# Kernel optimization log

Measured on AMD Instinct MI355X. Metric: run time of the kernel, lower is better.

## Reference

```python
import jax, jax.numpy as jnp
import numpy as np

NUM_HEADS = 16
HEAD_DIM = 64


def setup_inputs() -> dict:
    key = jax.random.key(0)
    ks = jax.random.split(key, 6)
    B, S, E = 4, 1024, 1024
    return {
        "x": jax.random.normal(ks[0], (B, S, E), dtype=jnp.float32),
        "W_qkv": jax.random.normal(ks[1], (E, 3 * E), dtype=jnp.float32) * 0.02,
        "b_qkv": jax.random.normal(ks[2], (3 * E,), dtype=jnp.float32) * 0.02,
        "pe": jax.random.normal(ks[3], (S, S, HEAD_DIM), dtype=jnp.float32) * 0.02,
        "W_out": jax.random.normal(ks[4], (E, E), dtype=jnp.float32) * 0.02,
        "b_out": jax.random.normal(ks[5], (E,), dtype=jnp.float32) * 0.02,
    }


def reference(x, W_qkv, b_qkv, pe, W_out, b_out):
    B, S, E = x.shape
    H, D = NUM_HEADS, HEAD_DIM
    scale = D ** -0.5
    # qkv projection: (B,S,3E) -> (3,B,H,S,D)
    qkv = (x @ W_qkv + b_qkv).reshape(B, S, 3, H, D).transpose(2, 0, 3, 1, 4)
    q, k, v = qkv[0], qkv[1], qkv[2]
    # raw scaled scores (NO softmax in original module)
    scores = jnp.einsum('bhxd,bhyd->bhxy', q, k) * scale
    # relative position bias: pe is (S,S,D) == (x,y,c); original permutes to (c,x,y)
    # then einsum('cxy,bnxc->bnxy', pe, q) -> equivalent to 'xyc,bhxc->bhxy'
    pe_q = jnp.einsum('xyc,bhxc->bhxy', pe, q) * scale
    attn = (scores + pe_q) @ v                      # (B,H,S,D)
    out = attn.transpose(0, 2, 1, 3).reshape(B, S, E)
    return out @ W_out + b_out
```

## Files before the change

### kernel.cpp

```cpp
#include <hip/hip_runtime.h>
#include <cstdint>
#include <cstddef>


typedef unsigned short u16;
typedef unsigned char  u8;
typedef __bf16 bf16x8 __attribute__((ext_vector_type(8)));
typedef float  f32x4  __attribute__((ext_vector_type(4)));
typedef unsigned short u16x8 __attribute__((ext_vector_type(8)));

#define MFMA16(a, b, c) __builtin_amdgcn_mfma_f32_16x16x32_bf16((a), (b), (c), 0, 0, 0)

#define GLOAD16(g, l)                                                        \
    __builtin_amdgcn_global_load_lds(                                        \
        (const __attribute__((address_space(1))) unsigned int*)(g),          \
        (__attribute__((address_space(3))) unsigned int*)(l), 16, 0, 0)

__device__ __forceinline__ u16 f2bf(float f) {
    __bf16 h = (__bf16)f;
    return __builtin_bit_cast(u16, h);
}
__device__ __forceinline__ u16x8 pack8(float4 a, float4 b) {
    u16x8 v;
    v[0] = f2bf(a.x); v[1] = f2bf(a.y); v[2] = f2bf(a.z); v[3] = f2bf(a.w);
    v[4] = f2bf(b.x); v[5] = f2bf(b.y); v[6] = f2bf(b.z); v[7] = f2bf(b.w);
    return v;
}

__device__ __forceinline__ void convT_tile(const float* __restrict__ in,
                                           u16* __restrict__ out, int R, int C,
                                           int bx, int by, float (*tile)[68]) {
    const int t  = threadIdx.x;
    const int r0 = by * 64, c0 = bx * 64;
    const int rr = t >> 4, c4 = t & 15;
    for (int p = 0; p < 4; ++p) {
        int r = rr + p * 16;
        float4 v = *(const float4*)&in[(size_t)(r0 + r) * C + c0 + c4 * 4];
        *(float4*)&tile[r][c4 * 4] = v;
    }
    __syncthreads();
    for (int p = 0; p < 4; ++p) {
        int n = rr + p * 16;
        ushort4 o;
        o.x = f2bf(tile[c4 * 4 + 0][n]);
        o.y = f2bf(tile[c4 * 4 + 1][n]);
        o.z = f2bf(tile[c4 * 4 + 2][n]);
        o.w = f2bf(tile[c4 * 4 + 3][n]);
        *(ushort4*)&out[(size_t)(c0 + n) * R + r0 + c4 * 4] = o;
    }
}

__global__ __launch_bounds__(256) void kprep(const float* __restrict__ x,
                                             u16* __restrict__ xb,
                                             const float* __restrict__ Wqkv,
                                             u16* __restrict__ wqkvT,
                                             const float* __restrict__ Wout,
                                             u16* __restrict__ woutT) {
    __shared__ float tile[64][68];
    const int bid = blockIdx.x;
    if (bid < 2048) {
        int i = (bid * 256 + threadIdx.x) * 8;
        float4 f0 = *(const float4*)&x[i];
        float4 f1 = *(const float4*)&x[i + 4];
        *(u16x8*)&xb[i] = pack8(f0, f1);
    } else if (bid < 2816) {
        int r = bid - 2048;
        convT_tile(Wqkv, wqkvT, 1024, 3072, r % 48, r / 48, tile);
    } else {
        int r = bid - 2816;
        convT_tile(Wout, woutT, 1024, 1024, r % 16, r / 16, tile);
    }
}

__global__ __launch_bounds__(256, 2) void kgemm_qkv(const u16* __restrict__ A,
                                                    const u16* __restrict__ WT,
                                                    const float* __restrict__ bias,
                                                    u16* __restrict__ qb,
                                                    u16* __restrict__ kb,
                                                    u16* __restrict__ vtb) {
    __shared__ u16 a_s[128 * 64];
    __shared__ u16 b_s[128 * 64];
    const int t = threadIdx.x;
    const int m0 = blockIdx.y * 128, n0 = blockIdx.x * 128;
    const int lane = t & 63, w = t >> 6, lm = lane & 15, lq = lane >> 4;
    const int mb = (w >> 1) * 64, nb = (w & 1) * 64;
    const int sr = t >> 3, sc = (t & 7) * 8;

    f32x4 acc[4][4] = {};
    for (int k0 = 0; k0 < 1024; k0 += 64) {
        __syncthreads();
#pragma unroll
        for (int p = 0; p < 4; ++p) {
            GLOAD16(&A [(size_t)(m0 + p * 32 + sr) * 1024 + k0 + sc], &a_s[p * 2048 + t * 8]);
            GLOAD16(&WT[(size_t)(n0 + p * 32 + sr) * 1024 + k0 + sc], &b_s[p * 2048 + t * 8]);
        }
        __syncthreads();
#pragma unroll
        for (int ks = 0; ks < 2; ++ks) {
            bf16x8 af[4], bfr[4];
#pragma unroll
            for (int mt = 0; mt < 4; ++mt)
                af[mt] = *(const bf16x8*)&a_s[(mb + mt * 16 + lm) * 64 + ks * 32 + lq * 8];
#pragma unroll
            for (int nt = 0; nt < 4; ++nt)
                bfr[nt] = *(const bf16x8*)&b_s[(nb + nt * 16 + lm) * 64 + ks * 32 + lq * 8];
#pragma unroll
            for (int mt = 0; mt < 4; ++mt)
#pragma unroll
                for (int nt = 0; nt < 4; ++nt)
                    acc[mt][nt] = MFMA16(af[mt], bfr[nt], acc[mt][nt]);
        }
    }
    for (int nt = 0; nt < 4; ++nt) {
        int col = n0 + nb + nt * 16 + lm;
        float bv = bias[col];
        int which = col >> 10;
        int h = (col >> 6) & 15, d = col & 63;
        for (int mt = 0; mt < 4; ++mt) {
            int row0 = m0 + mb + mt * 16 + lq * 4;
            int b = row0 >> 10, s = row0 & 1023;
            if (which == 2) {
                ushort4 o;
                o.x = f2bf(acc[mt][nt][0] + bv);
                o.y = f2bf(acc[mt][nt][1] + bv);
                o.z = f2bf(acc[mt][nt][2] + bv);
                o.w = f2bf(acc[mt][nt][3] + bv);
                *(ushort4*)&vtb[((size_t)(b * 16 + h) * 64 + d) * 1024 + s] = o;
            } else {
                u16* dst = (which == 0) ? qb : kb;
                for (int i = 0; i < 4; ++i)
                    dst[((size_t)((b * 16 + h) * 1024 + s + i)) * 64 + d] =
                        f2bf(acc[mt][nt][i] + bv);
            }
        }
    }
}

__global__ __launch_bounds__(256, 4) void kpq(const u16* __restrict__ qb,
                                              const float* __restrict__ pe,
                                              u8* __restrict__ Pq) {
    __shared__ u16 q_s[64 * 64];
    __shared__ u16 pe_s[64 * 80];
    __shared__ unsigned int o_s[64 * 17];
    const int x = blockIdx.x;
    const int t = threadIdx.x;
    const int lane = t & 63, w = t >> 6, lm = lane & 15, lq = lane >> 4;
#pragma unroll
    for (int p = 0; p < 2; ++p)
        GLOAD16(&qb[(size_t)((p * 32 + (t >> 3)) * 1024 + x) * 64 + (t & 7) * 8],
                &q_s[p * 2048 + t * 8]);
    const int yl = t >> 2, cq = (t & 3) * 16;
    const float* pex = pe + (size_t)x * 65536;
    float4 r0, r1, r2, r3;
    {
        const float* src = &pex[(size_t)yl * 64 + cq];
        r0 = *(const float4*)&src[0];  r1 = *(const float4*)&src[4];
        r2 = *(const float4*)&src[8];  r3 = *(const float4*)&src[12];
    }
    const int obh = t >> 2, oyc = t & 3;
    for (int it = 0; it < 16; ++it) {
        *(u16x8*)&pe_s[yl * 80 + cq]     = pack8(r0, r1);
        *(u16x8*)&pe_s[yl * 80 + cq + 8] = pack8(r2, r3);
        __syncthreads();
        if (it < 15) {
            const float* src = &pex[(size_t)((it + 1) * 64 + yl) * 64 + cq];
            r0 = *(const float4*)&src[0];  r1 = *(const float4*)&src[4];
            r2 = *(const float4*)&src[8];  r3 = *(const float4*)&src[12];
        }
        f32x4 acc[4] = {};
#pragma unroll
        for (int ks = 0; ks < 2; ++ks) {
            bf16x8 a = *(const bf16x8*)&pe_s[(16 * w + lm) * 80 + ks * 32 + lq * 8];
#pragma unroll
            for (int nt = 0; nt < 4; ++nt) {
                bf16x8 b = *(const bf16x8*)&q_s[(nt * 16 + lm) * 64 + ks * 32 + lq * 8];
                acc[nt] = MFMA16(a, b, acc[nt]);
            }
        }
#pragma unroll
        for (int nt = 0; nt < 4; ++nt) {
            unsigned int pw;
            pw = __builtin_amdgcn_cvt_pk_fp8_f32(acc[nt][0], acc[nt][1], 0u, false);
            pw = __builtin_amdgcn_cvt_pk_fp8_f32(acc[nt][2], acc[nt][3], pw, true);
            o_s[(nt * 16 + lm) * 17 + 4 * w + lq] = pw;
        }
        __syncthreads();
        uint4 dv;
        dv.x = o_s[obh * 17 + oyc * 4 + 0];
        dv.y = o_s[obh * 17 + oyc * 4 + 1];
        dv.z = o_s[obh * 17 + oyc * 4 + 2];
        dv.w = o_s[obh * 17 + oyc * 4 + 3];
        *(uint4*)&Pq[((size_t)obh * 1024 + x) * 1024 + it * 64 + oyc * 16] = dv;
    }
}

__global__ __launch_bounds__(256, 2) void kattn(const u16* __restrict__ qb,
                                                const u16* __restrict__ kb,
                                                const u16* __restrict__ vt,
                                                const u8* __restrict__ Pq,
                                                u16* __restrict__ attnb) {
    __shared__ u16 q_s[128 * 64];
    __shared__ u16 k_s[64 * 64];
    __shared__ u16 v_s[64 * 64];
    __shared__ u16 s_s[128 * 80];
    const int bid = blockIdx.x;
    const int bh = bid & 63, x0 = (bid >> 6) * 128;
    const int t = threadIdx.x;
    const int lane = t & 63, w = t >> 6, lm = lane & 15, lq = lane >> 4;
    const int sr = t >> 3, sc = (t & 7) * 8;

#pragma unroll
    for (int p = 0; p < 4; ++p)
        GLOAD16(&qb[(size_t)(bh * 1024 + x0 + p * 32 + sr) * 64 + sc],
                &q_s[p * 2048 + t * 8]);

    const u8* PqRow = Pq + ((size_t)(bh * 1024) + x0 + 32 * w + lm) * 1024 + lq * 4;
    f32x4 oacc[2][4] = {};
    for (int y0 = 0; y0 < 1024; y0 += 64) {
        unsigned int pqr[4][2];
#pragma unroll
        for (int nt = 0; nt < 2; ++nt)
#pragma unroll
            for (int mt = 0; mt < 4; ++mt)
                pqr[mt][nt] = *(const unsigned int*)&PqRow[(size_t)(nt * 16) * 1024 + y0 + mt * 16];
        __syncthreads();
#pragma unroll
        for (int p = 0; p < 2; ++p) {
            GLOAD16(&kb[(size_t)(bh * 1024 + y0 + p * 32 + sr) * 64 + sc],
                    &k_s[p * 2048 + t * 8]);
            GLOAD16(&vt[(size_t)(bh * 64 + p * 32 + sr) * 1024 + y0 + sc],
                    &v_s[p * 2048 + t * 8]);
        }
        __syncthreads();
        f32x4 sacc[4][2] = {};
#pragma unroll
        for (int ks = 0; ks < 2; ++ks) {
            bf16x8 bq[2];
#pragma unroll
            for (int nt = 0; nt < 2; ++nt)
                bq[nt] = *(const bf16x8*)&q_s[(32 * w + nt * 16 + lm) * 64 + ks * 32 + lq * 8];
#pragma unroll
            for (int mt = 0; mt < 4; ++mt) {
                bf16x8 ak = *(const bf16x8*)&k_s[(mt * 16 + lm) * 64 + ks * 32 + lq * 8];
#pragma unroll
                for (int nt = 0; nt < 2; ++nt)
                    sacc[mt][nt] = MFMA16(ak, bq[nt], sacc[mt][nt]);
            }
        }
#pragma unroll
        for (int nt = 0; nt < 2; ++nt) {
            int xl = 32 * w + nt * 16 + lm;
#pragma unroll
            for (int mt = 0; mt < 4; ++mt) {
                unsigned int pw = pqr[mt][nt];
                ushort4 o;
                o.x = f2bf((sacc[mt][nt][0] + __builtin_amdgcn_cvt_f32_fp8(pw, 0)) * 0.125f);
                o.y = f2bf((sacc[mt][nt][1] + __builtin_amdgcn_cvt_f32_fp8(pw, 1)) * 0.125f);
                o.z = f2bf((sacc[mt][nt][2] + __builtin_amdgcn_cvt_f32_fp8(pw, 2)) * 0.125f);
                o.w = f2bf((sacc[mt][nt][3] + __builtin_amdgcn_cvt_f32_fp8(pw, 3)) * 0.125f);
                *(ushort4*)&s_s[xl * 80 + mt * 16 + lq * 4] = o;
            }
        }
#pragma unroll
        for (int ks = 0; ks < 2; ++ks) {
            bf16x8 as[2];
#pragma unroll
            for (int mt = 0; mt < 2; ++mt)
                as[mt] = *(const bf16x8*)&s_s[(32 * w + mt * 16 + lm) * 80 + ks * 32 + lq * 8];
#pragma unroll
            for (int nt = 0; nt < 4; ++nt) {
                bf16x8 bv = *(const bf16x8*)&v_s[(nt * 16 + lm) * 64 + ks * 32 + lq * 8];
#pragma unroll
                for (int mt = 0; mt < 2; ++mt)
                    oacc[mt][nt] = MFMA16(as[mt], bv, oacc[mt][nt]);
            }
        }
    }
    const int b = bh >> 4, h = bh & 15;
    for (int mt = 0; mt < 2; ++mt) {
        for (int nt = 0; nt < 4; ++nt) {
            int d = nt * 16 + lm;
            for (int i = 0; i < 4; ++i) {
                int s = x0 + 32 * w + mt * 16 + lq * 4 + i;
                attnb[((size_t)(b * 1024 + s)) * 1024 + h * 64 + d] = f2bf(oacc[mt][nt][i]);
            }
        }
    }
}

__global__ __launch_bounds__(256, 2) void kgemm_out(const u16* __restrict__ A,
                                                    const u16* __restrict__ WT,
                                                    const float* __restrict__ bias,
                                                    float* __restrict__ out) {
    __shared__ u16 a_s[128 * 64];
    __shared__ u16 b_s[128 * 64];
    const int t = threadIdx.x;
    const int m0 = blockIdx.y * 128, n0 = blockIdx.x * 128;
    const int lane = t & 63, w = t >> 6, lm = lane & 15, lq = lane >> 4;
    const int mb = (w >> 1) * 64, nb = (w & 1) * 64;
    const int sr = t >> 3, sc = (t & 7) * 8;

    f32x4 acc[4][4] = {};
    for (int k0 = 0; k0 < 1024; k0 += 64) {
        __syncthreads();
#pragma unroll
        for (int p = 0; p < 4; ++p) {
            GLOAD16(&A [(size_t)(m0 + p * 32 + sr) * 1024 + k0 + sc], &a_s[p * 2048 + t * 8]);
            GLOAD16(&WT[(size_t)(n0 + p * 32 + sr) * 1024 + k0 + sc], &b_s[p * 2048 + t * 8]);
        }
        __syncthreads();
#pragma unroll
        for (int ks = 0; ks < 2; ++ks) {
            bf16x8 af[4], bfr[4];
#pragma unroll
            for (int mt = 0; mt < 4; ++mt)
                af[mt] = *(const bf16x8*)&a_s[(mb + mt * 16 + lm) * 64 + ks * 32 + lq * 8];
#pragma unroll
            for (int nt = 0; nt < 4; ++nt)
                bfr[nt] = *(const bf16x8*)&b_s[(nb + nt * 16 + lm) * 64 + ks * 32 + lq * 8];
#pragma unroll
            for (int mt = 0; mt < 4; ++mt)
#pragma unroll
                for (int nt = 0; nt < 4; ++nt)
                    acc[mt][nt] = MFMA16(af[mt], bfr[nt], acc[mt][nt]);
        }
    }
    for (int nt = 0; nt < 4; ++nt) {
        int col = n0 + nb + nt * 16 + lm;
        float bv = bias[col];
        for (int mt = 0; mt < 4; ++mt) {
            for (int i = 0; i < 4; ++i) {
                int row = m0 + mb + mt * 16 + lq * 4 + i;
                out[(size_t)row * 1024 + col] = acc[mt][nt][i] + bv;
            }
        }
    }
}

extern "C" void kernel_launch(void* const* d_in, const int* in_sizes, int n_in,
                              void* d_out, int out_size, void* d_ws, size_t ws_size,
                              hipStream_t stream) {
    (void)in_sizes; (void)n_in; (void)out_size; (void)ws_size;
    const float* x    = (const float*)d_in[0];
    const float* Wqkv = (const float*)d_in[1];
    const float* bqkv = (const float*)d_in[2];
    const float* pe   = (const float*)d_in[3];
    const float* Wout = (const float*)d_in[4];
    const float* bout = (const float*)d_in[5];
    float* out = (float*)d_out;

    char* ws = (char*)d_ws;
    u16* xb    = (u16*)ws;  ws += (size_t)4096 * 1024 * 2;
    u16* wqkvT = (u16*)ws;  ws += (size_t)3072 * 1024 * 2;
    u16* woutT = (u16*)ws;  ws += (size_t)1024 * 1024 * 2;
    u16* qb    = (u16*)ws;  ws += (size_t)64 * 1024 * 64 * 2;
    u16* kb    = (u16*)ws;  ws += (size_t)64 * 1024 * 64 * 2;
    u16* vtb   = (u16*)ws;  ws += (size_t)64 * 64 * 1024 * 2;
    u16* attnb = (u16*)ws;  ws += (size_t)4 * 1024 * 1024 * 2;
    u8*  pq    = (u8*)ws;   ws += (size_t)64 * 1024 * 1024;

    kprep<<<3072, 256, 0, stream>>>(x, xb, Wqkv, wqkvT, Wout, woutT);
    kgemm_qkv<<<dim3(24, 32), 256, 0, stream>>>(xb, wqkvT, bqkv, qb, kb, vtb);
    kpq<<<1024, 256, 0, stream>>>(qb, pe, pq);
    kattn<<<512, 256, 0, stream>>>(qb, kb, vtb, pq, attnb);
    kgemm_out<<<dim3(8, 32), 256, 0, stream>>>(attnb, woutT, bout, out);
}
```

Measured before the change: 530.3 us.

## Permute fp8 Pq layout so kpq writes directly and kattn uses 16-byte loads

Changes the in-memory order of the fp8 position-bias tensor Pq within each 64-column chunk, so the kpq kernel can write each lane's packed fp8 word straight to global memory. This removes the shared-memory transpose staging buffer and one barrier per iteration. pe_s is double-buffered so the remaining single barrier is enough to separate writes from reads. kattn is updated to match the new layout and now reads its per-lane Pq values with one 16-byte load instead of four 4-byte loads. The cost is that kpq now issues scattered 4-byte global stores instead of coalesced 16-byte ones.

```diff
diff --git a/kernel.cpp b/kernel.cpp
--- a/kernel.cpp
+++ b/kernel.cpp
@@ -140,8 +140,7 @@
                                               const float* __restrict__ pe,
                                               u8* __restrict__ Pq) {
     __shared__ u16 q_s[64 * 64];
-    __shared__ u16 pe_s[64 * 80];
-    __shared__ unsigned int o_s[64 * 17];
+    __shared__ u16 pe_s[2][64 * 80];
     const int x = blockIdx.x;
     const int t = threadIdx.x;
     const int lane = t & 63, w = t >> 6, lm = lane & 15, lq = lane >> 4;
@@ -157,10 +156,11 @@
         r0 = *(const float4*)&src[0];  r1 = *(const float4*)&src[4];
         r2 = *(const float4*)&src[8];  r3 = *(const float4*)&src[12];
     }
-    const int obh = t >> 2, oyc = t & 3;
+    u8* pq_base = Pq + ((size_t)lm * 1024 + x) * 1024 + lq * 16 + w * 4;
+    int cur = 0;
     for (int it = 0; it < 16; ++it) {
-        *(u16x8*)&pe_s[yl * 80 + cq]     = pack8(r0, r1);
-        *(u16x8*)&pe_s[yl * 80 + cq + 8] = pack8(r2, r3);
+        *(u16x8*)&pe_s[cur][yl * 80 + cq]     = pack8(r0, r1);
+        *(u16x8*)&pe_s[cur][yl * 80 + cq + 8] = pack8(r2, r3);
         __syncthreads();
         if (it < 15) {
             const float* src = &pex[(size_t)((it + 1) * 64 + yl) * 64 + cq];
@@ -170,7 +170,7 @@
         f32x4 acc[4] = {};
 #pragma unroll
         for (int ks = 0; ks < 2; ++ks) {
-            bf16x8 a = *(const bf16x8*)&pe_s[(16 * w + lm) * 80 + ks * 32 + lq * 8];
+            bf16x8 a = *(const bf16x8*)&pe_s[cur][(16 * w + lm) * 80 + ks * 32 + lq * 8];
 #pragma unroll
             for (int nt = 0; nt < 4; ++nt) {
                 bf16x8 b = *(const bf16x8*)&q_s[(nt * 16 + lm) * 64 + ks * 32 + lq * 8];
@@ -182,15 +182,9 @@
             unsigned int pw;
             pw = __builtin_amdgcn_cvt_pk_fp8_f32(acc[nt][0], acc[nt][1], 0u, false);
             pw = __builtin_amdgcn_cvt_pk_fp8_f32(acc[nt][2], acc[nt][3], pw, true);
-            o_s[(nt * 16 + lm) * 17 + 4 * w + lq] = pw;
-        }
-        __syncthreads();
-        uint4 dv;
-        dv.x = o_s[obh * 17 + oyc * 4 + 0];
-        dv.y = o_s[obh * 17 + oyc * 4 + 1];
-        dv.z = o_s[obh * 17 + oyc * 4 + 2];
-        dv.w = o_s[obh * 17 + oyc * 4 + 3];
-        *(uint4*)&Pq[((size_t)obh * 1024 + x) * 1024 + it * 64 + oyc * 16] = dv;
+            *(unsigned int*)&pq_base[(size_t)nt * 16 * 1024 * 1024 + it * 64] = pw;
+        }
+        cur ^= 1;
     }
 }
 
@@ -214,15 +208,13 @@
         GLOAD16(&qb[(size_t)(bh * 1024 + x0 + p * 32 + sr) * 64 + sc],
                 &q_s[p * 2048 + t * 8]);
 
-    const u8* PqRow = Pq + ((size_t)(bh * 1024) + x0 + 32 * w + lm) * 1024 + lq * 4;
+    const u8* PqRow = Pq + ((size_t)(bh * 1024) + x0 + 32 * w + lm) * 1024 + lq * 16;
     f32x4 oacc[2][4] = {};
     for (int y0 = 0; y0 < 1024; y0 += 64) {
-        unsigned int pqr[4][2];
+        uint4 pq4[2];
 #pragma unroll
         for (int nt = 0; nt < 2; ++nt)
-#pragma unroll
-            for (int mt = 0; mt < 4; ++mt)
-                pqr[mt][nt] = *(const unsigned int*)&PqRow[(size_t)(nt * 16) * 1024 + y0 + mt * 16];
+            pq4[nt] = *(const uint4*)&PqRow[(size_t)(nt * 16) * 1024 + y0];
         __syncthreads();
 #pragma unroll
         for (int p = 0; p < 2; ++p) {
@@ -250,9 +242,10 @@
 #pragma unroll
         for (int nt = 0; nt < 2; ++nt) {
             int xl = 32 * w + nt * 16 + lm;
+            const unsigned int* pqc = (const unsigned int*)&pq4[nt];
 #pragma unroll
             for (int mt = 0; mt < 4; ++mt) {
-                unsigned int pw = pqr[mt][nt];
+                unsigned int pw = pqc[mt];
                 ushort4 o;
                 o.x = f2bf((sacc[mt][nt][0] + __builtin_amdgcn_cvt_f32_fp8(pw, 0)) * 0.125f);
                 o.y = f2bf((sacc[mt][nt][1] + __builtin_amdgcn_cvt_f32_fp8(pw, 1)) * 0.125f);
```

Result: no change. 522.0 us (-1.5%).
